# Kernel optimization log

Hardware: AMD Instinct MI355X
Metric: run time of the kernel (lower is better)

## Reference

```python
import jax, jax.numpy as jnp
import numpy as np

BN_EPS = 1e-3  # keras BatchNormalization default epsilon


def _conv(x, w):
    # x: [B,H,W,Cin], w: [kh,kw,Cin,Cout], stride 1, SAME padding
    return jax.lax.conv_general_dilated(
        x, w, window_strides=(1, 1), padding='SAME',
        dimension_numbers=('NHWC', 'HWIO', 'NHWC'))


def _bn(x, g, b, m, v):
    return (x - m) * jax.lax.rsqrt(v + BN_EPS) * g + b


def _pam(x, wq, bq, wk, bk, wv, bv, gamma):
    # Position attention: softmax over HW x HW similarity of 1x1-conv q/k.
    B, H, W, C = x.shape
    q = (_conv(x, wq) + bq).reshape(B, H * W, -1)   # [B,HW,C/8]
    k = (_conv(x, wk) + bk).reshape(B, H * W, -1)   # [B,HW,C/8]
    v = (_conv(x, wv) + bv).reshape(B, H * W, C)    # [B,HW,C]
    energy = jnp.einsum('bic,bjc->bij', q, k)       # [B,HW,HW]
    att = jax.nn.softmax(energy, axis=-1)
    out = jnp.einsum('bij,bjc->bic', att, v).reshape(B, H, W, C)
    return gamma * out + x


def _cam(x, gamma):
    # Channel attention with max-subtract stabilization, softmax over C.
    B, H, W, C = x.shape
    X = x.reshape(B, H * W, C)                      # channel-last flat
    energy = jnp.einsum('bnc,bnd->bcd', X, X)       # [B,C,C]
    energy_new = jnp.max(energy, axis=-1, keepdims=True) - energy
    att = jax.nn.softmax(energy_new, axis=-1)       # [B,C,C]
    out = jnp.einsum('bcd,bnd->bnc', att, X).reshape(B, H, W, C)
    return gamma * out + x


def setup_inputs() -> dict:
    key = jax.random.key(0)
    ks = jax.random.split(key, 16)
    B, H, W = 4, 64, 64
    Cin, Ci, Cq, Cout = 512, 128, 16, 19
    s = 0.05
    d = {
        'x': jax.random.normal(ks[0], (B, H, W, Cin), jnp.float32),
        'w5a': jax.random.normal(ks[1], (3, 3, Cin, Ci), jnp.float32) * s,
        'w5c': jax.random.normal(ks[2], (3, 3, Cin, Ci), jnp.float32) * s,
        'wq': jax.random.normal(ks[3], (1, 1, Ci, Cq), jnp.float32) * s,
        'bq': jnp.zeros((Cq,), jnp.float32),
        'wk': jax.random.normal(ks[4], (1, 1, Ci, Cq), jnp.float32) * s,
        'bk': jnp.zeros((Cq,), jnp.float32),
        'wv': jax.random.normal(ks[5], (1, 1, Ci, Ci), jnp.float32) * s,
        'bv': jnp.zeros((Ci,), jnp.float32),
        'pam_gamma': jnp.float32(0.5),
        'cam_gamma': jnp.float32(0.5),
        'w51': jax.random.normal(ks[6], (3, 3, Ci, Ci), jnp.float32) * s,
        'w52': jax.random.normal(ks[7], (3, 3, Ci, Ci), jnp.float32) * s,
        'w8': jax.random.normal(ks[8], (1, 1, Ci, Cout), jnp.float32) * s,
    }
    for i, nm in enumerate(['bn1', 'bn2', 'bn3', 'bn4']):
        d[nm + '_g'] = jnp.ones((Ci,), jnp.float32)
        d[nm + '_b'] = jnp.zeros((Ci,), jnp.float32)
        d[nm + '_m'] = jax.random.normal(ks[9 + i], (Ci,), jnp.float32) * 0.1
        d[nm + '_v'] = jnp.ones((Ci,), jnp.float32)
    return d


def reference(x, w5a, w5c, wq, bq, wk, bk, wv, bv, pam_gamma, cam_gamma,
              w51, w52, w8,
              bn1_g, bn1_b, bn1_m, bn1_v,
              bn2_g, bn2_b, bn2_m, bn2_v,
              bn3_g, bn3_b, bn3_m, bn3_v,
              bn4_g, bn4_b, bn4_m, bn4_v):
    # PAM branch
    feat1 = jax.nn.relu(_bn(_conv(x, w5a), bn1_g, bn1_b, bn1_m, bn1_v))
    sa_feat = _pam(feat1, wq, bq, wk, bk, wv, bv, pam_gamma)
    sa_conv = jax.nn.relu(_bn(_conv(sa_feat, w51), bn3_g, bn3_b, bn3_m, bn3_v))
    # CAM branch
    feat2 = jax.nn.relu(_bn(_conv(x, w5c), bn2_g, bn2_b, bn2_m, bn2_v))
    sc_feat = _cam(feat2, cam_gamma)
    sc_conv = jax.nn.relu(_bn(_conv(sc_feat, w52), bn4_g, bn4_b, bn4_m, bn4_v))
    # Fused output (dropout is identity at inference)
    feat_sum = sa_conv + sc_conv
    return _conv(feat_sum, w8)
```

## Files before the change

kernel.cpp:

```cpp
#include <hip/hip_runtime.h>
#include <hip/hip_bf16.h>
#include <math.h>

#define BN_EPS 1e-3f

constexpr int Bn = 4, Hn = 64, Wn = 64, CIN = 512, CI = 128;
constexpr int HWn = Hn * Wn;
constexpr int NPIX = Bn * HWn;
constexpr int COn = 19;

struct F8 { float4 lo, hi; };

__device__ __forceinline__ F8 f8zero() {
    F8 r; r.lo = make_float4(0.f,0.f,0.f,0.f); r.hi = make_float4(0.f,0.f,0.f,0.f); return r;
}
__device__ __forceinline__ void fma8(F8 &acc, float a, const float4 &wlo, const float4 &whi) {
    acc.lo.x = fmaf(a, wlo.x, acc.lo.x);
    acc.lo.y = fmaf(a, wlo.y, acc.lo.y);
    acc.lo.z = fmaf(a, wlo.z, acc.lo.z);
    acc.lo.w = fmaf(a, wlo.w, acc.lo.w);
    acc.hi.x = fmaf(a, whi.x, acc.hi.x);
    acc.hi.y = fmaf(a, whi.y, acc.hi.y);
    acc.hi.z = fmaf(a, whi.z, acc.hi.z);
    acc.hi.w = fmaf(a, whi.w, acc.hi.w);
}

typedef __attribute__((ext_vector_type(8)))  short    short8;
typedef __attribute__((ext_vector_type(8)))  _Float16 half8;
typedef __attribute__((ext_vector_type(16))) float    f32x16;

__device__ __forceinline__ f32x16 f16z() {
    f32x16 z;
    #pragma unroll
    for (int i = 0; i < 16; ++i) z[i] = 0.f;
    return z;
}
__device__ __forceinline__ unsigned f2b(float f) {
    union { float f; unsigned u; } c; c.f = f;
    return (c.u + 0x7FFFu + ((c.u >> 16) & 1u)) >> 16;
}
__device__ __forceinline__ unsigned pack2(float lo, float hi) {
    return (f2b(hi) << 16) | f2b(lo);
}
__device__ __forceinline__ void split2(float a, float b, unsigned &hi, unsigned &lo) {
    const unsigned ha = f2b(a), hb = f2b(b);
    union { unsigned u; float f; } ua, ub; ua.u = ha << 16; ub.u = hb << 16;
    hi = (hb << 16) | ha;
    lo = pack2(a - ua.f, b - ub.f);
}
__device__ __forceinline__ unsigned pkh2(float a, float b) {
    union { _Float16 h; unsigned short u; } ca, cb;
    ca.h = (_Float16)a; cb.h = (_Float16)b;
    return ((unsigned)cb.u << 16) | ca.u;
}

__global__ __launch_bounds__(256)
void k_prep_w(const float* __restrict__ w5a, const float* __restrict__ w5c,
              const float* __restrict__ w51, const float* __restrict__ w52,
              char* __restrict__ wt1F, char* __restrict__ wt2aF, char* __restrict__ wt2bF)
{
    int idx = blockIdx.x * 256 + threadIdx.x;
    if (idx < 589824) {
        const int jp = idx & 7, co = (idx >> 3) & 255, ct = idx >> 11;
        const int tap = ct % 9, c = ct / 9;
        const float* src = (co < 128) ? w5a : w5c;
        const int coc = co & 127;
        const int ci = c*16 + jp*2;
        const float a = src[((size_t)tap*CIN + ci)*CI + coc];
        const float b = src[((size_t)tap*CIN + ci + 1)*CI + coc];
        const int L = co*32 + jp*4;
        *(unsigned*)(wt1F + (size_t)ct*8192 + L) = pkh2(a, b);
    } else {
        int k = idx - 589824;
        if (k >= 147456) return;
        const float* src = (k < 73728) ? w51 : w52;
        char* dstF = (k < 73728) ? wt2aF : wt2bF;
        if (k >= 73728) k -= 73728;
        const int jp = k & 7, co = (k >> 3) & 127, ct = k >> 10;
        const int tap = ct % 9, c = ct / 9;
        const int ci = c*16 + jp*2;
        const float a = src[((size_t)tap*CI + ci)*CI + co];
        const float b = src[((size_t)tap*CI + ci + 1)*CI + co];
        const int L = co*32 + jp*4;
        *(unsigned*)(dstF + (size_t)ct*4096 + L) = pkh2(a, b);
    }
}

__global__ __launch_bounds__(256)
void k_prep_bn(const float* g1, const float* b1, const float* m1, const float* v1,
               const float* g2, const float* b2, const float* m2, const float* v2,
               const float* g3, const float* b3, const float* m3, const float* v3,
               const float* g4, const float* b4, const float* m4, const float* v4,
               float* bnAs, float* bnAb, float* bnBs, float* bnBb)
{
    const int t = threadIdx.x, c = t & 127;
    {
        const float *g = (t < 128) ? g1 : g2, *b = (t < 128) ? b1 : b2;
        const float *m = (t < 128) ? m1 : m2, *v = (t < 128) ? v1 : v2;
        const float s = g[c] * rsqrtf(v[c] + BN_EPS);
        bnAs[t] = s; bnAb[t] = b[c] - m[c]*s;
    }
    {
        const float *g = (t < 128) ? g3 : g4, *b = (t < 128) ? b3 : b4;
        const float *m = (t < 128) ? m3 : m4, *v = (t < 128) ? v3 : v4;
        const float s = g[c] * rsqrtf(v[c] + BN_EPS);
        bnBs[t] = s; bnBb[t] = b[c] - m[c]*s;
    }
}

__global__ __launch_bounds__(256)
void k_prep_x(const float* __restrict__ x, _Float16* __restrict__ xcv)
{
    __shared__ float Xl[16*520];
    const int t = threadIdx.x;
    const int pb = blockIdx.x * 16;
    #pragma unroll
    for (int i = 0; i < 8; ++i) {
        const int u = t + i*256;
        const int px = u >> 7, c4 = (u & 127) * 4;
        *(float4*)&Xl[px*520 + c4] = *(const float4*)&x[(size_t)(pb + px)*CIN + c4];
    }
    __syncthreads();
    const int rowg = pb >> 6, pixb = pb & 63;
    #pragma unroll
    for (int i = 0; i < 8; ++i) {
        const int u = t + i*256;
        const int chunk = u >> 6, rem = u & 63;
        const int pl = rem >> 2, u4 = rem & 3;
        const float* src = &Xl[pl*520 + chunk*16 + u4*4];
        uint2 v;
        v.x = pkh2(src[0], src[1]);
        v.y = pkh2(src[2], src[3]);
        *(uint2*)&xcv[(((size_t)rowg*32 + chunk)*64 + (pixb + pl))*16 + u4*4] = v;
    }
}

template<int NCHNK, int NCOTOT, int WCOBASE>
__global__ __launch_bounds__(256)
void k_convh(const _Float16* __restrict__ xcv0, const _Float16* __restrict__ xcv1,
             const _Float16* __restrict__ wtF0, const _Float16* __restrict__ wtF1,
             const float* __restrict__ bnS, const float* __restrict__ bnBi,
             float* __restrict__ out0, float* __restrict__ out1)
{
    constexpr int XPAGE = 66*32;
    constexpr int XCH   = 3*XPAGE;
    __shared__ __align__(16) char Xs[2*2*XCH];

    const int t    = threadIdx.x;
    const int wgid = blockIdx.x;
    const int xcd  = wgid & 7;
    const int sel  = xcd >> 2;
    const int ch2  = (xcd >> 1) & 1;
    const int row  = ((wgid >> 3) << 1) | (xcd & 1);
    const _Float16* xcv = sel ? xcv1 : xcv0;
    const _Float16* wtF = sel ? wtF1 : wtF0;
    float* dst = sel ? out1 : out0;

    const int hh = row & 63;
    const int dyLo = (hh == 0)  ? 1 : 0;
    const int dyHi = (hh == 63) ? 1 : 2;
    const int l = t & 63, w = t >> 6;
    const int lo5 = l & 31, hf = l >> 5;
    const int mi = w >> 1, nt = w & 1;
    const int corow = WCOBASE*sel + ch2*64 + nt*32 + lo5;

    bool sAct[7], sIn[7]; int sLoff[7]; unsigned sGoff[7];
    #pragma unroll
    for (int i = 0; i < 7; ++i) {
        const int u = t + i*256;
        sAct[i] = false; sIn[i] = false; sLoff[i] = 0; sGoff[i] = 0;
        if (u < 1584) {
            const int cc = (u >= 792) ? 1 : 0;
            const int uu = u - cc*792;
            const int dyr = uu/264, rs = uu - dyr*264;
            const int s = rs >> 2, u4 = rs & 3;
            sAct[i]  = (dyr >= dyLo && dyr <= dyHi);
            sIn[i]   = (s >= 1 && s <= 64);
            sLoff[i] = cc*XCH + dyr*XPAGE + ((s*32 + u4*8) ^ ((s & 7) << 4));
            sGoff[i] = (unsigned)(((row + dyr - 1)*NCHNK + cc)*1024 + (s - 1)*16 + u4*4);
        }
    }
    int xoff[3];
    #pragma unroll
    for (int dx = 0; dx < 3; ++dx) {
        const int s = mi*32 + lo5 + dx;
        xoff[dx] = (s*32 + hf*16) ^ ((s & 7) << 4);
    }

    f32x16 acc = f16z();
    half8 wA[9], wB[9];

    auto issueW9 = [&](int c, half8 (&wr)[9]) {
        #pragma unroll
        for (int tap = 0; tap < 9; ++tap)
            wr[tap] = *(const half8*)&wtF[((size_t)(c*9 + tap)*NCOTOT + corow)*16 + hf*8];
    };
    auto compC = [&](const char* Xb, int cc, const half8 (&wr)[9]) {
        #pragma unroll
        for (int dy = 0; dy < 3; ++dy) {
            if (dy < dyLo || dy > dyHi) continue;
            const char* Xp = Xb + cc*XCH + dy*XPAGE;
            #pragma unroll
            for (int dx = 0; dx < 3; ++dx) {
                const half8 xf = *(const half8*)(Xp + xoff[dx]);
                acc = __builtin_amdgcn_mfma_f32_32x32x16_f16(wr[dy*3 + dx], xf, acc, 0, 0, 0);
            }
        }
    };

    uint2 xr[7];
    auto loadX = [&](int cbase) {
        #pragma unroll
        for (int i = 0; i < 7; ++i) {
            uint2 v; v.x = 0u; v.y = 0u;
            if (sAct[i] && sIn[i])
                v = *(const uint2*)&xcv[(size_t)sGoff[i] + (size_t)cbase*1024];
            xr[i] = v;
        }
    };

    loadX(0);
    int p = 0;
    for (int c = 0; c < NCHNK; c += 2) {
        issueW9(c, wA);
        char* Xb = Xs + p*2*XCH;
        #pragma unroll
        for (int i = 0; i < 7; ++i)
            if (sAct[i]) *(uint2*)(Xb + sLoff[i]) = xr[i];
        __syncthreads();
        if (c + 2 < NCHNK) loadX(c + 2);
        issueW9(c + 1, wB);
        compC(Xb, 0, wA);
        compC(Xb, 1, wB);
        p ^= 1;
    }
    const int px = mi*32 + lo5;
    const size_t pg = (size_t)row*Wn + px;
    #pragma unroll
    for (int r = 0; r < 16; ++r) {
        const int crow = (r & 3) + 8*(r >> 2) + 4*hf;
        const int och = ch2*64 + nt*32 + crow;
        const int bnidx = sel*128 + och;
        dst[pg*CI + och] = fmaxf(fmaf(acc[r], bnS[bnidx], bnBi[bnidx]), 0.f);
    }
}

__global__ __launch_bounds__(256)
void k_qk(const float* __restrict__ feat1,
          const float* __restrict__ wq, const float* __restrict__ bq,
          const float* __restrict__ wk, const float* __restrict__ bk,
          __hip_bfloat16* __restrict__ qb, __hip_bfloat16* __restrict__ kb)
{
    __shared__ float Al[64*129];
    __shared__ __align__(16) float Wl[128*32];
    const int t = threadIdx.x;
    const int pb = blockIdx.x * 64;
    for (int idx = t; idx < 64*128; idx += 256) {
        const int p = idx >> 7, ci = idx & 127;
        Al[p*129 + ci] = feat1[(size_t)(pb + p)*CI + ci];
    }
    for (int idx = t; idx < 128*32; idx += 256) {
        const int ci = idx >> 5, c = idx & 31;
        Wl[idx] = (c < 16) ? wq[ci*16 + c] : wk[ci*16 + (c - 16)];
    }
    __syncthreads();
    const int p = t & 63, cg = t >> 6, co = cg * 8;
    F8 acc = f8zero();
    #pragma unroll 8
    for (int ci = 0; ci < 128; ++ci) {
        const float a = Al[p*129 + ci];
        const float4 wlo = *(const float4*)&Wl[ci*32 + co];
        const float4 whi = *(const float4*)&Wl[ci*32 + co + 4];
        fma8(acc, a, wlo, whi);
    }
    const float* af = (const float*)&acc;
    #pragma unroll
    for (int j = 0; j < 8; ++j) {
        const int c = co + j;
        if (c < 16) qb[(size_t)(pb + p)*16 + c]        = __float2bfloat16(af[j] + bq[c]);
        else        kb[(size_t)(pb + p)*16 + (c - 16)] = __float2bfloat16(af[j] + bk[c - 16]);
    }
}

__global__ __launch_bounds__(256)
void k_v(const float* __restrict__ feat1, const float* __restrict__ wv,
         const float* __restrict__ bv, __hip_bfloat16* __restrict__ vbT)
{
    __shared__ float Al[32*129];
    __shared__ __align__(16) float Wl[64*128];
    const int t = threadIdx.x;
    const int pb = blockIdx.x * 32;
    for (int idx = t; idx < 32*128; idx += 256) {
        const int p = idx >> 7, ci = idx & 127;
        Al[p*129 + ci] = feat1[(size_t)(pb + p)*CI + ci];
    }
    const int px = t & 15, co = (t >> 4) * 8;
    F8 acc0 = f8zero(), acc1 = f8zero();
    for (int ch = 0; ch < 2; ++ch) {
        __syncthreads();
        #pragma unroll
        for (int r = 0; r < 8; ++r) {
            const int i4 = t + r*256;
            const int kk = i4 >> 5, c4 = (i4 & 31) * 4;
            *(float4*)&Wl[kk*128 + c4] = *(const float4*)&wv[(size_t)(ch*64 + kk)*CI + c4];
        }
        __syncthreads();
        #pragma unroll 4
        for (int kk = 0; kk < 64; ++kk) {
            const float a0 = Al[px*129 + ch*64 + kk];
            const float a1 = Al[(px+16)*129 + ch*64 + kk];
            const float4 wlo = *(const float4*)&Wl[kk*128 + co];
            const float4 whi = *(const float4*)&Wl[kk*128 + co + 4];
            fma8(acc0, a0, wlo, whi);
            fma8(acc1, a1, wlo, whi);
        }
    }
    const int p0 = pb + px;
    const int bb = p0 / HWn, pin0 = p0 % HWn;
    const float* a0f = (const float*)&acc0;
    const float* a1f = (const float*)&acc1;
    #pragma unroll
    for (int j = 0; j < 8; ++j) {
        const int c = co + j;
        const size_t rowb = ((size_t)bb*CI + c) * HWn;
        vbT[rowb + pin0]      = __float2bfloat16(a0f[j] + bv[c]);
        vbT[rowb + pin0 + 16] = __float2bfloat16(a1f[j] + bv[c]);
    }
}

__global__ __launch_bounds__(256)
void k_pam(const __hip_bfloat16* __restrict__ qb, const __hip_bfloat16* __restrict__ kb,
           const __hip_bfloat16* __restrict__ vbT, const float* __restrict__ feat1,
           const float* __restrict__ gamma, _Float16* __restrict__ saf_h)
{
    __shared__ __align__(16) char pbuf[16896];
    __shared__ float msArr[4][32];
    __shared__ float ssArr[4][32];
    __shared__ float ssum[32];
    const int t  = threadIdx.x;
    const int wv = t >> 6, l = t & 63;
    const int lo5 = l & 31, h = l >> 5;
    unsigned* Ppk = (unsigned*)(pbuf + wv*4096);
    float* osum = (float*)pbuf;

    const int q0 = blockIdx.x * 32;
    const int bb = q0 / HWn;
    const size_t jb = (size_t)bb * HWn;
    const __hip_bfloat16* vbB = vbT + (size_t)bb * CI * HWn;

    const short8 qfrag = *(const short8*)&qb[(size_t)(q0 + lo5)*16 + 8*h];
    const f32x16 zro = f16z();

    f32x16 o[4];
    #pragma unroll
    for (int cb = 0; cb < 4; ++cb) o[cb] = f16z();

    float m_run = -1e30f, s_run = 0.f;

    for (int k0 = wv*1024; k0 < wv*1024 + 1024; k0 += 64) {
        const short8 kf0 = *(const short8*)&kb[(jb + k0 +      lo5)*16 + 8*h];
        const short8 kf1 = *(const short8*)&kb[(jb + k0 + 32 + lo5)*16 + 8*h];
        short8 vf[4][4];
        #pragma unroll
        for (int s = 0; s < 4; ++s)
            #pragma unroll
            for (int cb = 0; cb < 4; ++cb)
                vf[s][cb] = *(const short8*)&vbB[((size_t)(cb*32 + lo5))*HWn + k0 + s*16 + 8*h];

        f32x16 e0 = __builtin_amdgcn_mfma_f32_32x32x16_bf16(kf0, qfrag, zro, 0, 0, 0);
        f32x16 e1 = __builtin_amdgcn_mfma_f32_32x32x16_bf16(kf1, qfrag, zro, 0, 0, 0);

        float mt = fmaxf(e0[0], e1[0]);
        #pragma unroll
        for (int r = 1; r < 16; ++r) mt = fmaxf(mt, fmaxf(e0[r], e1[r]));
        mt = fmaxf(mt, __shfl_xor(mt, 32));

        if (__any(mt > m_run + 8.f)) {
            const float mnew = fmaxf(m_run, mt);
            const float sc = __expf(m_run - mnew);
            s_run *= sc;
            #pragma unroll
            for (int cb = 0; cb < 4; ++cb)
                #pragma unroll
                for (int r = 0; r < 16; ++r) o[cb][r] *= sc;
            m_run = mnew;
        }

        #pragma unroll
        for (int r = 0; r < 16; ++r) {
            e0[r] = __expf(e0[r] - m_run);
            e1[r] = __expf(e1[r] - m_run);
        }
        float ss = 0.f;
        #pragma unroll
        for (int r = 0; r < 16; ++r) ss += e0[r] + e1[r];
        s_run += ss;

        #pragma unroll
        for (int r = 0; r < 16; r += 2) {
            const int pidx = ((r & 3) >> 1) + 4*(r >> 2) + 2*h;
            Ppk[pidx*32 + lo5]        = pack2(e0[r], e0[r+1]);
            Ppk[(16 + pidx)*32 + lo5] = pack2(e1[r], e1[r+1]);
        }
        #pragma unroll
        for (int s = 0; s < 4; ++s) {
            union { unsigned u[4]; short8 s8; } P;
            #pragma unroll
            for (int w = 0; w < 4; ++w)
                P.u[w] = Ppk[(s*8 + 4*h + w)*32 + lo5];
            #pragma unroll
            for (int cb = 0; cb < 4; ++cb)
                o[cb] = __builtin_amdgcn_mfma_f32_32x32x16_bf16(vf[s][cb], P.s8, o[cb], 0, 0, 0);
        }
    }

    const float s_w = s_run + __shfl_xor(s_run, 32);
    if (h == 0) { msArr[wv][lo5] = m_run; ssArr[wv][lo5] = s_w; }
    __syncthreads();

    float M = msArr[0][lo5];
    #pragma unroll
    for (int w = 1; w < 4; ++w) M = fmaxf(M, msArr[w][lo5]);
    float stot = 0.f;
    #pragma unroll
    for (int w = 0; w < 4; ++w) stot += __expf(msArr[w][lo5] - M) * ssArr[w][lo5];
    if (wv == 0 && h == 0) ssum[lo5] = stot;
    const float myscale = __expf(m_run - M);
    #pragma unroll
    for (int cb = 0; cb < 4; ++cb)
        #pragma unroll
        for (int r = 0; r < 16; ++r) o[cb][r] *= myscale;

    for (int w = 0; w < 4; ++w) {
        if (wv == w) {
            #pragma unroll
            for (int cb = 0; cb < 4; ++cb)
                #pragma unroll
                for (int r = 0; r < 16; ++r) {
                    const int c = cb*32 + (r & 3) + 8*(r >> 2) + 4*h;
                    float* p = &osum[lo5*132 + c];
                    if (w == 0) *p = o[cb][r]; else *p += o[cb][r];
                }
        }
        __syncthreads();
    }

    const float g = gamma[0];
    const int qloc = t >> 3, ch8 = t & 7;
    const float inv = 1.f / ssum[qloc];
    const int pgl = q0 + qloc;
    const int rowp = pgl >> 6, pixp = pgl & 63;
    const size_t gbase = (size_t)pgl*CI + ch8*16;
    union { _Float16 hv[16]; uint4 u[2]; } tmp;
    #pragma unroll
    for (int j = 0; j < 16; ++j)
        tmp.hv[j] = (_Float16)(g*(osum[qloc*132 + ch8*16 + j]*inv) + feat1[gbase + j]);
    uint4* dsth = (uint4*)&saf_h[((size_t)(rowp*8 + ch8)*64 + pixp)*16];
    dsth[0] = tmp.u[0];
    dsth[1] = tmp.u[1];
}

__global__ __launch_bounds__(256)
void k_xpose(const float* __restrict__ feat2,
             char* __restrict__ f2TH, char* __restrict__ f2TL)
{
    __shared__ float Xl[64*129];
    const int t = threadIdx.x;
    const int pb = blockIdx.x * 64;
    const int bb = pb / HWn, pin = pb % HWn;
    for (int idx = t; idx < 64*128; idx += 256) {
        const int p = idx >> 7, ci = idx & 127;
        Xl[p*129 + ci] = feat2[(size_t)(pb + p)*CI + ci];
    }
    __syncthreads();
    const int c = t >> 1, half = t & 1;
    const size_t rowb = ((size_t)(bb*CI + c)*HWn + pin + half*32) * 2;
    #pragma unroll
    for (int j = 0; j < 16; ++j) {
        const float a = Xl[(half*32 + 2*j)*129 + c];
        const float b = Xl[(half*32 + 2*j + 1)*129 + c];
        unsigned hi, lo; split2(a, b, hi, lo);
        *(unsigned*)(f2TH + rowb + 4*j) = hi;
        *(unsigned*)(f2TL + rowb + 4*j) = lo;
    }
}

__global__ __launch_bounds__(256)
void k_cam_energy_m(const char* __restrict__ f2TH, const char* __restrict__ f2TL,
                    float* __restrict__ epart)
{
    __shared__ __align__(16) char Vh[128*256];
    __shared__ __align__(16) char Vl[128*256];
    const int t = threadIdx.x;
    const int ks = blockIdx.x, bb = blockIdx.y;
    const int l = t & 63, w = t >> 6;
    const int lo5 = l & 31, hf = l >> 5;

    #pragma unroll
    for (int pass = 0; pass < 8; ++pass) {
        const int slot = pass*256 + t;
        const int c = slot >> 4, g = slot & 15;
        const size_t gaddr = ((size_t)(bb*CI + c)*HWn + ks*128)*2 + g*16;
        const int laddr = c*256 + ((g*16) ^ ((c & 15) << 4));
        *(float4*)(Vh + laddr) = *(const float4*)(f2TH + gaddr);
        *(float4*)(Vl + laddr) = *(const float4*)(f2TL + gaddr);
    }
    __syncthreads();

    f32x16 acc[4];
    #pragma unroll
    for (int nj = 0; nj < 4; ++nj) acc[nj] = f16z();
    const int cA = w*32 + lo5;
    const int swA = (cA & 15) << 4;

    #pragma unroll
    for (int kk = 0; kk < 8; ++kk) {
        const int kb = kk*32 + hf*16;
        const short8 ah = *(const short8*)(Vh + cA*256 + (kb ^ swA));
        const short8 al = *(const short8*)(Vl + cA*256 + (kb ^ swA));
        #pragma unroll
        for (int nj = 0; nj < 4; ++nj) {
            const int dB = nj*32 + lo5;
            const int swB = (dB & 15) << 4;
            const short8 bh = *(const short8*)(Vh + dB*256 + (kb ^ swB));
            const short8 bl = *(const short8*)(Vl + dB*256 + (kb ^ swB));
            acc[nj] = __builtin_amdgcn_mfma_f32_32x32x16_bf16(ah, bh, acc[nj], 0, 0, 0);
            acc[nj] = __builtin_amdgcn_mfma_f32_32x32x16_bf16(al, bh, acc[nj], 0, 0, 0);
            acc[nj] = __builtin_amdgcn_mfma_f32_32x32x16_bf16(ah, bl, acc[nj], 0, 0, 0);
        }
    }
    float* ep = epart + ((size_t)(bb*32 + ks)*CI)*CI;
    #pragma unroll
    for (int nj = 0; nj < 4; ++nj)
        #pragma unroll
        for (int r = 0; r < 16; ++r) {
            const int c = w*32 + (r & 3) + 8*(r >> 2) + 4*hf;
            ep[(size_t)c*CI + nj*32 + lo5] = acc[nj][r];
        }
}

__global__ __launch_bounds__(64)
void k_cam_rs(const float* __restrict__ epart, float* __restrict__ att)
{
    const int lane = threadIdx.x;
    const int row = blockIdx.x;
    const int bb = row >> 7, c = row & 127;
    float2 e = make_float2(0.f, 0.f);
    for (int ks = 0; ks < 32; ++ks) {
        const float2 v = *(const float2*)&epart[
            ((size_t)(bb*32 + ks)*CI + c)*CI + lane*2];
        e.x += v.x; e.y += v.y;
    }
    float M = fmaxf(e.x, e.y);
    #pragma unroll
    for (int off = 32; off > 0; off >>= 1) M = fmaxf(M, __shfl_xor(M, off));
    const float en0 = M - e.x, en1 = M - e.y;
    float mx = fmaxf(en0, en1);
    #pragma unroll
    for (int off = 32; off > 0; off >>= 1) mx = fmaxf(mx, __shfl_xor(mx, off));
    const float p0 = __expf(en0 - mx), p1 = __expf(en1 - mx);
    float s = p0 + p1;
    #pragma unroll
    for (int off = 32; off > 0; off >>= 1) s += __shfl_xor(s, off);
    const float inv = 1.f / s;
    float2 o; o.x = p0*inv; o.y = p1*inv;
    *(float2*)&att[(size_t)row*CI + lane*2] = o;
}

__global__ __launch_bounds__(256)
void k_cam_apply(const float* __restrict__ feat2, const float* __restrict__ att,
                 const float* __restrict__ gamma, _Float16* __restrict__ scf_h)
{
    __shared__ float Xl[64*129];
    __shared__ __align__(16) float aT[128*64];
    const int t = threadIdx.x;
    const int pb = blockIdx.x * 64;
    const int bb = pb / HWn;
    const int ch = blockIdx.y * 64;
    for (int idx = t; idx < 64*128; idx += 256) {
        const int p = idx >> 7, ci = idx & 127;
        Xl[p*129 + ci] = feat2[(size_t)(pb + p)*CI + ci];
    }
    for (int idx = t; idx < 128*64; idx += 256) {
        const int d = idx >> 6, cc = idx & 63;
        aT[d*64 + cc] = att[((size_t)bb*CI + ch + cc)*CI + d];
    }
    __syncthreads();
    const int px = t & 63, cg = t >> 6;
    F8 accA = f8zero(), accB = f8zero();
    #pragma unroll 4
    for (int d = 0; d < 128; ++d) {
        const float xv = Xl[px*129 + d];
        const float* ap = &aT[d*64 + cg*16];
        const float4 a0 = *(const float4*)&ap[0];
        const float4 a1 = *(const float4*)&ap[4];
        const float4 a2 = *(const float4*)&ap[8];
        const float4 a3 = *(const float4*)&ap[12];
        fma8(accA, xv, a0, a1);
        fma8(accB, xv, a2, a3);
    }
    const float g = gamma[0];
    const float* fa = (const float*)&accA;
    const float* fb = (const float*)&accB;
    const int p0g = pb + px;
    const int rowA = p0g >> 6, pixA = p0g & 63;
    const int chunkA = (ch >> 4) + cg;
    const size_t baseA = ((size_t)(rowA*8 + chunkA)*64 + pixA)*16;
    #pragma unroll
    for (int j = 0; j < 8; ++j) {
        const int cA = ch + cg*16 + j;
        const int cB = cA + 8;
        scf_h[baseA + j]     = (_Float16)(g*fa[j] + Xl[px*129 + cA]);
        scf_h[baseA + 8 + j] = (_Float16)(g*fb[j] + Xl[px*129 + cB]);
    }
}

__global__ __launch_bounds__(256)
void k_final(const float* __restrict__ sa, const float* __restrict__ sc,
             const float* __restrict__ w8, float* __restrict__ out)
{
    __shared__ float Xl[64*129];
    __shared__ float w8l[128*COn];
    const int t = threadIdx.x;
    const int pb = blockIdx.x * 64;
    for (int idx = t; idx < 64*128; idx += 256) {
        const int p = idx >> 7, ci = idx & 127;
        const size_t gi = (size_t)(pb + p)*CI + ci;
        Xl[p*129 + ci] = sa[gi] + sc[gi];
    }
    for (int idx = t; idx < 128*COn; idx += 256) w8l[idx] = w8[idx];
    __syncthreads();
    for (int idx = t; idx < 64*COn; idx += 256) {
        const int p = idx / COn, co = idx - p*COn;
        float acc = 0.f;
        #pragma unroll 8
        for (int ci = 0; ci < 128; ++ci)
            acc = fmaf(Xl[p*129 + ci], w8l[ci*COn + co], acc);
        out[(size_t)(pb + p)*COn + co] = acc;
    }
}

extern "C" void kernel_launch(void* const* d_in, const int* in_sizes, int n_in,
                              void* d_out, int out_size, void* d_ws, size_t ws_size,
                              hipStream_t stream)
{
    const float* x    = (const float*)d_in[0];
    const float* w5a  = (const float*)d_in[1];
    const float* w5c  = (const float*)d_in[2];
    const float* wq   = (const float*)d_in[3];
    const float* bq   = (const float*)d_in[4];
    const float* wk   = (const float*)d_in[5];
    const float* bk   = (const float*)d_in[6];
    const float* wv   = (const float*)d_in[7];
    const float* bv   = (const float*)d_in[8];
    const float* pgam = (const float*)d_in[9];
    const float* cgam = (const float*)d_in[10];
    const float* w51  = (const float*)d_in[11];
    const float* w52  = (const float*)d_in[12];
    const float* w8   = (const float*)d_in[13];
    const float* bn1g = (const float*)d_in[14];
    const float* bn1b = (const float*)d_in[15];
    const float* bn1m = (const float*)d_in[16];
    const float* bn1v = (const float*)d_in[17];
    const float* bn2g = (const float*)d_in[18];
    const float* bn2b = (const float*)d_in[19];
    const float* bn2m = (const float*)d_in[20];
    const float* bn2v = (const float*)d_in[21];
    const float* bn3g = (const float*)d_in[22];
    const float* bn3b = (const float*)d_in[23];
    const float* bn3m = (const float*)d_in[24];
    const float* bn3v = (const float*)d_in[25];
    const float* bn4g = (const float*)d_in[26];
    const float* bn4b = (const float*)d_in[27];
    const float* bn4m = (const float*)d_in[28];
    const float* bn4v = (const float*)d_in[29];

    char* wsb = (char*)d_ws;
    float* feat1 = (float*)(wsb + 0);
    char*  f2TH  = wsb + 0;
    char*  f2TL  = wsb + 4194304;
    float* feat2 = (float*)(wsb + 8388608);
    _Float16* xcv   = (_Float16*)(wsb + 16777216);
    _Float16* saf_h = (_Float16*)(wsb + 16777216);
    _Float16* scf_h = (_Float16*)(wsb + 20971520);
    float*    epart = (float*)(wsb + 25165824);
    float* att = (float*)(wsb + 33816576);
    __hip_bfloat16* qb16 = (__hip_bfloat16*)(wsb + 34078720);
    __hip_bfloat16* kb16 = (__hip_bfloat16*)(wsb + 34603008);
    __hip_bfloat16* vbT  = (__hip_bfloat16*)(wsb + 35127296);
    char* wt1F  = wsb + 39321600;
    char* wt2aF = wsb + 41680896;
    char* wt2bF = wsb + 41975808;
    float* bnAs = (float*)(wsb + 42270720);
    float* bnAb = (float*)(wsb + 42271744);
    float* bnBs = (float*)(wsb + 42272768);
    float* bnBb = (float*)(wsb + 42273792);
    float* sa_conv = feat1;
    float* sc_conv = feat2;
    float* out  = (float*)d_out;

    k_prep_w<<<dim3(2880), 256, 0, stream>>>(w5a, w5c, w51, w52, wt1F, wt2aF, wt2bF);
    k_prep_bn<<<dim3(1), 256, 0, stream>>>(bn1g, bn1b, bn1m, bn1v, bn2g, bn2b, bn2m, bn2v,
                                           bn3g, bn3b, bn3m, bn3v, bn4g, bn4b, bn4m, bn4v,
                                           bnAs, bnAb, bnBs, bnBb);
    k_prep_x<<<dim3(1024), 256, 0, stream>>>(x, xcv);
    k_convh<32, 256, 128><<<dim3(1024), 256, 0, stream>>>(
        xcv, xcv, (const _Float16*)wt1F, (const _Float16*)wt1F, bnAs, bnAb, feat1, feat2);
    k_qk<<<dim3(NPIX/64), 256, 0, stream>>>(feat1, wq, bq, wk, bk, qb16, kb16);
    k_v<<<dim3(NPIX/32), 256, 0, stream>>>(feat1, wv, bv, vbT);
    k_pam<<<dim3(NPIX/32), 256, 0, stream>>>(qb16, kb16, vbT, feat1, pgam, saf_h);
    k_xpose<<<dim3(NPIX/64), 256, 0, stream>>>(feat2, f2TH, f2TL);
    k_cam_energy_m<<<dim3(32, Bn), 256, 0, stream>>>(f2TH, f2TL, epart);
    k_cam_rs<<<dim3(Bn*CI), 64, 0, stream>>>(epart, att);
    k_cam_apply<<<dim3(NPIX/64, 2), 256, 0, stream>>>(feat2, att, cgam, scf_h);
    k_convh<8, 128, 0><<<dim3(1024), 256, 0, stream>>>(
        saf_h, scf_h, (const _Float16*)wt2aF, (const _Float16*)wt2bF,
        bnBs, bnBb, sa_conv, sc_conv);
    k_final<<<dim3(NPIX/64), 256, 0, stream>>>(sa_conv, sc_conv, w8, out);
}
```

Before: 244.2 us.

## Split PAM key range over eight waves and use exp2 softmax

```diff
diff --git a/kernel.cpp b/kernel.cpp
--- a/kernel.cpp
+++ b/kernel.cpp
@@ -3,6 +3,7 @@
 #include <math.h>
 
 #define BN_EPS 1e-3f
+#define LOG2E 1.44269504088896f
 
 constexpr int Bn = 4, Hn = 64, Wn = 64, CIN = 512, CI = 128;
 constexpr int HWn = Hn * Wn;
@@ -41,6 +42,11 @@
 }
 __device__ __forceinline__ unsigned pack2(float lo, float hi) {
     return (f2b(hi) << 16) | f2b(lo);
+}
+__device__ __forceinline__ unsigned pkb2(float a, float b) {
+    __hip_bfloat16 ha = __float2bfloat16(a);
+    __hip_bfloat16 hb = __float2bfloat16(b);
+    return ((unsigned)*(unsigned short*)&hb << 16) | *(unsigned short*)&ha;
 }
 __device__ __forceinline__ void split2(float a, float b, unsigned &hi, unsigned &lo) {
     const unsigned ha = f2b(a), hb = f2b(b);
@@ -277,7 +283,7 @@
     #pragma unroll
     for (int j = 0; j < 8; ++j) {
         const int c = co + j;
-        if (c < 16) qb[(size_t)(pb + p)*16 + c]        = __float2bfloat16(af[j] + bq[c]);
+        if (c < 16) qb[(size_t)(pb + p)*16 + c]        = __float2bfloat16((af[j] + bq[c]) * LOG2E);
         else        kb[(size_t)(pb + p)*16 + (c - 16)] = __float2bfloat16(af[j] + bk[c - 16]);
     }
 }
@@ -328,14 +334,14 @@
     }
 }
 
-__global__ __launch_bounds__(256)
+__global__ __launch_bounds__(512, 4)
 void k_pam(const __hip_bfloat16* __restrict__ qb, const __hip_bfloat16* __restrict__ kb,
            const __hip_bfloat16* __restrict__ vbT, const float* __restrict__ feat1,
            const float* __restrict__ gamma, _Float16* __restrict__ saf_h)
 {
-    __shared__ __align__(16) char pbuf[16896];
-    __shared__ float msArr[4][32];
-    __shared__ float ssArr[4][32];
+    __shared__ __align__(16) char pbuf[32768];
+    __shared__ float msArr[8][32];
+    __shared__ float ssArr[8][32];
     __shared__ float ssum[32];
     const int t  = threadIdx.x;
     const int wv = t >> 6, l = t & 63;
@@ -357,15 +363,9 @@
 
     float m_run = -1e30f, s_run = 0.f;
 
-    for (int k0 = wv*1024; k0 < wv*1024 + 1024; k0 += 64) {
+    for (int k0 = wv*512; k0 < wv*512 + 512; k0 += 64) {
         const short8 kf0 = *(const short8*)&kb[(jb + k0 +      lo5)*16 + 8*h];
         const short8 kf1 = *(const short8*)&kb[(jb + k0 + 32 + lo5)*16 + 8*h];
-        short8 vf[4][4];
-        #pragma unroll
-        for (int s = 0; s < 4; ++s)
-            #pragma unroll
-            for (int cb = 0; cb < 4; ++cb)
-                vf[s][cb] = *(const short8*)&vbB[((size_t)(cb*32 + lo5))*HWn + k0 + s*16 + 8*h];
 
         f32x16 e0 = __builtin_amdgcn_mfma_f32_32x32x16_bf16(kf0, qfrag, zro, 0, 0, 0);
         f32x16 e1 = __builtin_amdgcn_mfma_f32_32x32x16_bf16(kf1, qfrag, zro, 0, 0, 0);
@@ -375,9 +375,9 @@
         for (int r = 1; r < 16; ++r) mt = fmaxf(mt, fmaxf(e0[r], e1[r]));
         mt = fmaxf(mt, __shfl_xor(mt, 32));
 
-        if (__any(mt > m_run + 8.f)) {
+        if (__any(mt > m_run + 11.5416f)) {
             const float mnew = fmaxf(m_run, mt);
-            const float sc = __expf(m_run - mnew);
+            const float sc = exp2f(m_run - mnew);
             s_run *= sc;
             #pragma unroll
             for (int cb = 0; cb < 4; ++cb)
@@ -388,8 +388,8 @@
 
         #pragma unroll
         for (int r = 0; r < 16; ++r) {
-            e0[r] = __expf(e0[r] - m_run);
-            e1[r] = __expf(e1[r] - m_run);
+            e0[r] = exp2f(e0[r] - m_run);
+            e1[r] = exp2f(e1[r] - m_run);
         }
         float ss = 0.f;
         #pragma unroll
@@ -399,8 +399,8 @@
         #pragma unroll
         for (int r = 0; r < 16; r += 2) {
             const int pidx = ((r & 3) >> 1) + 4*(r >> 2) + 2*h;
-            Ppk[pidx*32 + lo5]        = pack2(e0[r], e0[r+1]);
-            Ppk[(16 + pidx)*32 + lo5] = pack2(e1[r], e1[r+1]);
+            Ppk[pidx*32 + lo5]        = pkb2(e0[r], e0[r+1]);
+            Ppk[(16 + pidx)*32 + lo5] = pkb2(e1[r], e1[r+1]);
         }
         #pragma unroll
         for (int s = 0; s < 4; ++s) {
@@ -409,8 +409,11 @@
             for (int w = 0; w < 4; ++w)
                 P.u[w] = Ppk[(s*8 + 4*h + w)*32 + lo5];
             #pragma unroll
-            for (int cb = 0; cb < 4; ++cb)
-                o[cb] = __builtin_amdgcn_mfma_f32_32x32x16_bf16(vf[s][cb], P.s8, o[cb], 0, 0, 0);
+            for (int cb = 0; cb < 4; ++cb) {
+                const short8 vf = *(const short8*)&vbB[
+                    ((size_t)(cb*32 + lo5))*HWn + k0 + s*16 + 8*h];
+                o[cb] = __builtin_amdgcn_mfma_f32_32x32x16_bf16(vf, P.s8, o[cb], 0, 0, 0);
+            }
         }
     }
 
@@ -420,18 +423,18 @@
 
     float M = msArr[0][lo5];
     #pragma unroll
-    for (int w = 1; w < 4; ++w) M = fmaxf(M, msArr[w][lo5]);
+    for (int w = 1; w < 8; ++w) M = fmaxf(M, msArr[w][lo5]);
     float stot = 0.f;
     #pragma unroll
-    for (int w = 0; w < 4; ++w) stot += __expf(msArr[w][lo5] - M) * ssArr[w][lo5];
+    for (int w = 0; w < 8; ++w) stot += exp2f(msArr[w][lo5] - M) * ssArr[w][lo5];
     if (wv == 0 && h == 0) ssum[lo5] = stot;
-    const float myscale = __expf(m_run - M);
+    const float myscale = exp2f(m_run - M);
     #pragma unroll
     for (int cb = 0; cb < 4; ++cb)
         #pragma unroll
         for (int r = 0; r < 16; ++r) o[cb][r] *= myscale;
 
-    for (int w = 0; w < 4; ++w) {
+    for (int w = 0; w < 8; ++w) {
         if (wv == w) {
             #pragma unroll
             for (int cb = 0; cb < 4; ++cb)
@@ -446,18 +449,17 @@
     }
 
     const float g = gamma[0];
-    const int qloc = t >> 3, ch8 = t & 7;
+    const int qloc = t >> 4, ch8 = t & 15;
     const float inv = 1.f / ssum[qloc];
     const int pgl = q0 + qloc;
     const int rowp = pgl >> 6, pixp = pgl & 63;
-    const size_t gbase = (size_t)pgl*CI + ch8*16;
-    union { _Float16 hv[16]; uint4 u[2]; } tmp;
-    #pragma unroll
-    for (int j = 0; j < 16; ++j)
-        tmp.hv[j] = (_Float16)(g*(osum[qloc*132 + ch8*16 + j]*inv) + feat1[gbase + j]);
-    uint4* dsth = (uint4*)&saf_h[((size_t)(rowp*8 + ch8)*64 + pixp)*16];
-    dsth[0] = tmp.u[0];
-    dsth[1] = tmp.u[1];
+    const int chunk = ch8 >> 1, intra = (ch8 & 1) * 8;
+    const size_t gbase = (size_t)pgl*CI + ch8*8;
+    union { _Float16 hv[8]; uint4 u; } tmp;
+    #pragma unroll
+    for (int j = 0; j < 8; ++j)
+        tmp.hv[j] = (_Float16)(g*(osum[qloc*132 + ch8*8 + j]*inv) + feat1[gbase + j]);
+    *(uint4*)&saf_h[((size_t)(rowp*8 + chunk)*64 + pixp)*16 + intra] = tmp.u;
 }
 
 __global__ __launch_bounds__(256)
@@ -708,7 +710,7 @@
         xcv, xcv, (const _Float16*)wt1F, (const _Float16*)wt1F, bnAs, bnAb, feat1, feat2);
     k_qk<<<dim3(NPIX/64), 256, 0, stream>>>(feat1, wq, bq, wk, bk, qb16, kb16);
     k_v<<<dim3(NPIX/32), 256, 0, stream>>>(feat1, wv, bv, vbT);
-    k_pam<<<dim3(NPIX/32), 256, 0, stream>>>(qb16, kb16, vbT, feat1, pgam, saf_h);
+    k_pam<<<dim3(NPIX/32), 512, 0, stream>>>(qb16, kb16, vbT, feat1, pgam, saf_h);
     k_xpose<<<dim3(NPIX/64), 256, 0, stream>>>(feat2, f2TH, f2TL);
     k_cam_energy_m<<<dim3(32, Bn), 256, 0, stream>>>(f2TH, f2TL, epart);
     k_cam_rs<<<dim3(Bn*CI), 64, 0, stream>>>(epart, att);
```

Result: slower. 271.8 us (+11.3%).
